# Performance work log

Hardware: AMD Instinct MI355X
Metric: run time of the kernel (lower is better)

The kernel has to match this reference:

```python
import jax, jax.numpy as jnp
import numpy as np
from functools import partial

K = 3
P = K * K * K          # 27 kernel points
G = 2                  # groups
PAD = 1
STRIDE = 1
DIL = 1
AXIS_SCALE = (0.5, 1.0, 1.0)   # (x, y, z) offset axis scale
CUR_SCALE = 0.5                # warmup scale at global_step=0
EPS = 1e-5


def setup_inputs() -> dict:
    key = jax.random.key(0)
    ks = jax.random.split(key, 8)
    C, OC = 64, 64
    N, D, H, W = 1, 32, 32, 32
    inp = {
        "x": jax.random.normal(ks[0], (N, C, D, H, W), jnp.float32),
        "dw_w": jax.random.normal(ks[1], (C, 1, K, K, K), jnp.float32) * 0.1,
        "gn_w": jnp.ones((C,), jnp.float32),
        "gn_b": jnp.zeros((C,), jnp.float32),
        "inp_w": jax.random.normal(ks[2], (C, C), jnp.float32) * (1.0 / np.sqrt(C)),
        "inp_b": jnp.zeros((C,), jnp.float32),
        # offset/mask weights are zero-init in the module; use small random values
        # so the deformable sampling path is exercised nontrivially.
        "off_w": jax.random.normal(ks[3], (C, G * P * 3), jnp.float32) * 0.01,
        "off_b": jnp.zeros((G * P * 3,), jnp.float32),
        "mask_w": jax.random.normal(ks[4], (C, G * P), jnp.float32) * 0.01,
        "mask_b": jnp.tile(jnp.full((P,), -5.0, jnp.float32).at[P // 2].set(0.0), (G,)),
        "out_w": jax.random.normal(ks[5], (C, OC), jnp.float32) * (1.0 / np.sqrt(C)),
        "out_b": jnp.zeros((OC,), jnp.float32),
    }
    return inp


def _trilinear(vol, loc):
    # vol: [Dp, Hp, Wp, gc]; loc: [..., 3] with (x, y, z) in [-1, 1]
    # grid_sample semantics: align_corners=False, padding_mode='zeros'
    Dp, Hp, Wp, _ = vol.shape
    ix = (loc[..., 0] + 1.0) * 0.5 * Wp - 0.5
    iy = (loc[..., 1] + 1.0) * 0.5 * Hp - 0.5
    iz = (loc[..., 2] + 1.0) * 0.5 * Dp - 0.5
    x0f, y0f, z0f = jnp.floor(ix), jnp.floor(iy), jnp.floor(iz)
    fx, fy, fz = ix - x0f, iy - y0f, iz - z0f
    x0, y0, z0 = x0f.astype(jnp.int32), y0f.astype(jnp.int32), z0f.astype(jnp.int32)
    out = jnp.zeros(loc.shape[:-1] + (vol.shape[-1],), vol.dtype)
    for dz in (0, 1):
        wz = fz if dz else 1.0 - fz
        cz = z0 + dz
        for dy in (0, 1):
            wy = fy if dy else 1.0 - fy
            cy = y0 + dy
            for dx in (0, 1):
                wx = fx if dx else 1.0 - fx
                cx = x0 + dx
                valid = ((cz >= 0) & (cz < Dp) & (cy >= 0) & (cy < Hp)
                         & (cx >= 0) & (cx < Wp))
                v = vol[jnp.clip(cz, 0, Dp - 1),
                        jnp.clip(cy, 0, Hp - 1),
                        jnp.clip(cx, 0, Wp - 1)]  # [..., gc]
                out = out + (wz * wy * wx * valid.astype(vol.dtype))[..., None] * v
    return out


def _forward(x, dw_w, gn_w, gn_b, inp_w, inp_b, off_w, off_b,
             mask_w, mask_b, out_w, out_b):
    N, C, D, H, W = x.shape
    gc = C // G
    # --- dw_conv: depthwise conv3d + GroupNorm(1, C) + GELU ---
    xc = jax.lax.conv_general_dilated(
        x, dw_w, window_strides=(1, 1, 1), padding=[(PAD, PAD)] * 3,
        dimension_numbers=("NCDHW", "OIDHW", "NCDHW"), feature_group_count=C)
    mu = xc.mean(axis=(1, 2, 3, 4), keepdims=True)
    var = ((xc - mu) ** 2).mean(axis=(1, 2, 3, 4), keepdims=True)
    xn = (xc - mu) * jax.lax.rsqrt(var + EPS)
    xn = xn * gn_w[None, :, None, None, None] + gn_b[None, :, None, None, None]
    x1 = jnp.transpose(jax.nn.gelu(xn), (0, 2, 3, 4, 1))       # [N,D,H,W,C]
    # --- offset / mask / input projection ---
    offset = x1 @ off_w + off_b                                  # [N,D,H,W,G*P*3]
    mask = jax.nn.softmax(
        (x1 @ mask_w + mask_b).reshape(N, D, H, W, G, P), axis=-1)
    xp = jnp.transpose(x, (0, 2, 3, 4, 1)) @ inp_w + inp_b       # [N,D,H,W,C]
    # --- core deformable sampling ---
    x_pad = jnp.pad(xp, ((0, 0), (PAD, PAD), (PAD, PAD), (PAD, PAD), (0, 0)))
    Dp, Hp, Wp = D + 2 * PAD, H + 2 * PAD, W + 2 * PAD
    Do = (D + 2 * PAD - DIL * (K - 1) - 1) // STRIDE + 1
    Ho = (H + 2 * PAD - DIL * (K - 1) - 1) // STRIDE + 1
    Wo = (W + 2 * PAD - DIL * (K - 1) - 1) // STRIDE + 1
    # reference grid (x/Wp, y/Hp, z/Dp)
    zc, yc, xc_ = jnp.meshgrid(jnp.arange(Do, dtype=jnp.float32),
                               jnp.arange(Ho, dtype=jnp.float32),
                               jnp.arange(Wo, dtype=jnp.float32), indexing="ij")
    ref = jnp.stack(((xc_ * STRIDE + PAD + 0.5) / Wp,
                     (yc * STRIDE + PAD + 0.5) / Hp,
                     (zc * STRIDE + PAD + 0.5) / Dp), axis=-1)   # [Do,Ho,Wo,3]
    # kernel grid
    lin = jnp.linspace(-(K - 1) // 2, (K - 1) // 2, K, dtype=jnp.float32)
    kz, ky, kx = jnp.meshgrid(lin, lin, lin, indexing="ij")
    kgrid = jnp.stack((kx * DIL / Wp, ky * DIL / Hp, kz * DIL / Dp),
                      axis=-1).reshape(P, 3)
    off = offset.reshape(N, Do, Ho, Wo, G, P, 3)
    off_norm = off / jnp.array([Wp, Hp, Dp], jnp.float32)
    axis = jnp.array(AXIS_SCALE, jnp.float32)
    loc = (ref[None, :, :, :, None, None, :]
           + kgrid[None, None, None, None, None, :, :]
           + off_norm * axis * CUR_SCALE)
    loc = loc * 2.0 - 1.0                                        # [N,Do,Ho,Wo,G,P,3]
    vol = jnp.transpose(x_pad.reshape(N, Dp, Hp, Wp, G, gc),
                        (0, 4, 1, 2, 3, 5))                      # [N,G,Dp,Hp,Wp,gc]
    locs = jnp.transpose(loc, (0, 4, 1, 2, 3, 5, 6))             # [N,G,Do,Ho,Wo,P,3]
    sampled = jax.vmap(jax.vmap(_trilinear))(vol, locs)          # [N,G,Do,Ho,Wo,P,gc]
    out = jnp.einsum("ngdhwpc,ndhwgp->ndhwgc", sampled, mask)
    out = out.reshape(N, Do, Ho, Wo, C)
    return out @ out_w + out_b                                   # [N,Do,Ho,Wo,OC]


def reference(x, dw_w, gn_w, gn_b, inp_w, inp_b, off_w, off_b,
              mask_w, mask_b, out_w, out_b):
    return _forward(x, dw_w, gn_w, gn_b, inp_w, inp_b, off_w, off_b,
                    mask_w, mask_b, out_w, out_b)
```

## Files before the change

kernel.cpp:

```cpp
#include <hip/hip_runtime.h>
#include <hip/hip_fp16.h>
#include <math.h>

#define SP 32768
#define PW 38
#define PW2 (PW*PW)
#define PVOX (PW*PW*PW)
#define OMS 228

typedef short bf16x8 __attribute__((ext_vector_type(8)));
typedef unsigned short u16x4 __attribute__((ext_vector_type(4)));
typedef float f32x4 __attribute__((ext_vector_type(4)));

__device__ __forceinline__ unsigned short f2b(float f) {
    unsigned u = __float_as_uint(f);
    u = (u + 0x7FFFu + ((u >> 16) & 1u)) >> 16;
    return (unsigned short)u;
}
__device__ __forceinline__ float b2f1(unsigned short s) {
    return __uint_as_float(((unsigned)s) << 16);
}
__device__ __forceinline__ __half2 h2(unsigned u) {
    return *reinterpret_cast<__half2*>(&u);
}
__device__ __forceinline__ int vox_of(int sb, int v) {
    int tw = sb & 7, th = (sb >> 3) & 15, td = sb >> 7;
    int vw = v & 3, vh = (v >> 2) & 1, vd = v >> 3;
    return (((td << 1) + vd) << 10) + (((th << 1) + vh) << 5) + (tw << 2) + vw;
}

__global__ void k_front(const float* __restrict__ x, const float* __restrict__ dw,
                        const float* __restrict__ off_w, const float* __restrict__ mask_w,
                        const float* __restrict__ off_b, const float* __restrict__ mask_b,
                        const float* __restrict__ inp_w, const float* __restrict__ out_w,
                        unsigned short* __restrict__ WcatB, float* __restrict__ bcat,
                        unsigned short* __restrict__ inpB, unsigned short* __restrict__ outB,
                        unsigned short* __restrict__ xcb, float* __restrict__ partials,
                        unsigned short* __restrict__ xpad) {
    int bb = blockIdx.x, tid = threadIdx.x;
    if (bb < 88) {
        int idx = bb * 256 + tid;
        int j = idx >> 6, k = idx & 63;
        if (j < 224) {
            float v = 0.f;
            if (j < 162) v = off_w[k * 162 + j];
            else if (j < 216) v = mask_w[k * 54 + (j - 162)];
            WcatB[j * 64 + k] = f2b(v);
            if (k == 0) bcat[j] = (j < 162) ? off_b[j] : (j < 216 ? mask_b[j - 162] : 0.f);
        } else if (j < 288) {
            outB[(j - 224) * 64 + k] = f2b(out_w[k * 64 + (j - 224)]);
        } else {
            inpB[(j - 288) * 64 + k] = f2b(inp_w[k * 64 + (j - 288)]);
        }
        return;
    }
    if (bb < 2136) {
        int b4 = bb - 88;
        int e4 = b4 * 256 + tid;
        int c = e4 >> 13, s4 = (e4 & 8191) << 2;
        int d = s4 >> 10, h = (s4 >> 5) & 31, w0 = s4 & 31;
        const float* xs = x + (size_t)c * SP;
        const float* wt = dw + c * 27;
        float a0 = 0.f, a1 = 0.f, a2 = 0.f, a3 = 0.f;
#pragma unroll
        for (int kd = 0; kd < 3; ++kd) {
            int zz = d + kd - 1; if ((unsigned)zz >= 32u) continue;
#pragma unroll
            for (int kh = 0; kh < 3; ++kh) {
                int yy = h + kh - 1; if ((unsigned)yy >= 32u) continue;
                const float* row = xs + (zz << 10) + (yy << 5) + w0;
                float4 L = *(const float4*)row;
                float xl = (w0 > 0) ? row[-1] : 0.f;
                float xr = (w0 < 28) ? row[4] : 0.f;
                const float* wr = wt + kd * 9 + kh * 3;
                float wm = wr[0], wc = wr[1], wp = wr[2];
                a0 = __builtin_fmaf(wm, xl,  __builtin_fmaf(wc, L.x, __builtin_fmaf(wp, L.y, a0)));
                a1 = __builtin_fmaf(wm, L.x, __builtin_fmaf(wc, L.y, __builtin_fmaf(wp, L.z, a1)));
                a2 = __builtin_fmaf(wm, L.y, __builtin_fmaf(wc, L.z, __builtin_fmaf(wp, L.w, a2)));
                a3 = __builtin_fmaf(wm, L.z, __builtin_fmaf(wc, L.w, __builtin_fmaf(wp, xr,  a3)));
            }
        }
        u16x4 o4; o4[0] = f2b(a0); o4[1] = f2b(a1); o4[2] = f2b(a2); o4[3] = f2b(a3);
        *(u16x4*)(xcb + (size_t)e4 * 4) = o4;
        float s1 = a0 + a1 + a2 + a3;
        float s2 = a0 * a0 + a1 * a1 + a2 * a2 + a3 * a3;
#pragma unroll
        for (int off = 32; off > 0; off >>= 1) {
            s1 += __shfl_xor(s1, off);
            s2 += __shfl_xor(s2, off);
        }
        __shared__ float ws[8];
        int wv = tid >> 6, lane = tid & 63;
        if (lane == 0) { ws[wv * 2] = s1; ws[wv * 2 + 1] = s2; }
        __syncthreads();
        if (tid == 0) {
            partials[b4 * 2 + 0] = ws[0] + ws[2] + ws[4] + ws[6];
            partials[b4 * 2 + 1] = ws[1] + ws[3] + ws[5] + ws[7];
        }
        return;
    }
    int cblk = bb - 2136;
    int j = tid >> 4, c4 = tid & 15;
    u16x4 z = {0, 0, 0, 0};
#pragma unroll
    for (int k = 0; k < 4; ++k) {
        int v = cblk * 64 + k * 16 + j;
        if (v >= PVOX) break;
        int zz = v / PW2, r = v - zz * PW2, yy = r / PW, xx = r - yy * PW;
        if (zz < 2 || zz > 33 || yy < 2 || yy > 33 || xx < 2 || xx > 33)
            *(u16x4*)(xpad + (size_t)v * 64 + c4 * 4) = z;
    }
}

__global__ void k_mid(const unsigned short* __restrict__ xcb, const float* __restrict__ partials,
                      const float* __restrict__ gn_w, const float* __restrict__ gn_b,
                      unsigned short* __restrict__ x1b,
                      const float* __restrict__ x,
                      const unsigned short* __restrict__ inpB,
                      const float* __restrict__ inp_b,
                      unsigned short* __restrict__ xpad) {
    int bb = blockIdx.x, tid = threadIdx.x;
    if (bb < 512) {
        __shared__ float rs[256], rq[256];
        __shared__ unsigned short tile[64][66];
        float a = 0.f, b = 0.f;
        for (int i = tid; i < 2048; i += 256) { a += partials[2 * i]; b += partials[2 * i + 1]; }
        rs[tid] = a; rq[tid] = b;
        __syncthreads();
        for (int off = 128; off > 0; off >>= 1) {
            if (tid < off) { rs[tid] += rs[tid + off]; rq[tid] += rq[tid + off]; }
            __syncthreads();
        }
        const float Minv = 1.f / 2097152.f;
        float mu = rs[0] * Minv;
        float var = rq[0] * Minv - mu * mu;
        float rsq = rsqrtf(var + 1e-5f);
        int s0 = bb * 64;
        int row = tid >> 6, lane = tid & 63;
        for (int c = row; c < 64; c += 4) {
            float v = (b2f1(xcb[(size_t)c * SP + s0 + lane]) - mu) * rsq * gn_w[c] + gn_b[c];
            float t2 = 1.5957691216057308f * (v + 0.044715f * v * v * v);
            tile[c][lane] = f2b(v / (1.f + __expf(-t2)));
        }
        __syncthreads();
        for (int r = row; r < 64; r += 4)
            x1b[(size_t)(s0 + r) * 64 + lane] = tile[lane][r];
        return;
    }
    {
        __shared__ unsigned short tileT[64][72];
        int s0b = (bb - 512) * 64;
        int row = tid >> 6, lane = tid & 63;
        for (int c = row; c < 64; c += 4)
            tileT[lane][c] = f2b(x[(size_t)c * SP + s0b + lane]);
        __syncthreads();
        int wv = row, quad = lane >> 4, col = lane & 15;
        int s0 = s0b + wv * 16;
        bf16x8 a0 = *(const bf16x8*)(&tileT[wv * 16 + col][quad * 8]);
        bf16x8 a1 = *(const bf16x8*)(&tileT[wv * 16 + col][32 + quad * 8]);
        int vp[4];
#pragma unroll
        for (int r = 0; r < 4; ++r) {
            int s = s0 + (quad << 2) + r;
            vp[r] = (((s >> 10) + 2) * PW + ((s >> 5) & 31) + 2) * PW + (s & 31) + 2;
        }
#pragma unroll
        for (int nt = 0; nt < 4; ++nt) {
            int n0 = nt * 16;
            bf16x8 b0 = *(const bf16x8*)(inpB + (n0 + col) * 64 + quad * 8);
            bf16x8 b1 = *(const bf16x8*)(inpB + (n0 + col) * 64 + 32 + quad * 8);
            f32x4 c = {0.f, 0.f, 0.f, 0.f};
            c = __builtin_amdgcn_mfma_f32_16x16x32_bf16(a0, b0, c, 0, 0, 0);
            c = __builtin_amdgcn_mfma_f32_16x16x32_bf16(a1, b1, c, 0, 0, 0);
            float bq = inp_b[n0 + col];
#pragma unroll
            for (int r = 0; r < 4; ++r)
                xpad[(size_t)vp[r] * 64 + n0 + col] =
                    __half_as_ushort(__float2half(c[r] + bq));
        }
    }
}

template<int P0, int NP>
__device__ __forceinline__ void sampleN(const float* __restrict__ orow,
                                        const float* __restrict__ mrow,
                                        const char* __restrict__ volc,
                                        float xb, float yb, float zb,
                                        float* __restrict__ acc) {
#pragma unroll
    for (int i = 0; i < NP; ++i) {
        const int p = P0 + i;
        const int px = p % 3, py = (p / 3) % 3, pz = p / 9;
        float ox = orow[p * 3 + 0], oy = orow[p * 3 + 1], oz = orow[p * 3 + 2];
        float mk = mrow[p];
        float ix = __builtin_fmaf(0.25f, ox, xb + (float)px);
        float iy = __builtin_fmaf(0.5f, oy, yb + (float)py);
        float iz = __builtin_fmaf(0.5f, oz, zb + (float)pz);
        ix = fminf(fmaxf(ix, 0.f), 36.f);
        iy = fminf(fmaxf(iy, 0.f), 36.f);
        iz = fminf(fmaxf(iz, 0.f), 36.f);
        float xf = floorf(ix), yf = floorf(iy), zf = floorf(iz);
        float fx = ix - xf, fy = iy - yf, fz = iz - zf;
        float fi = __builtin_fmaf(zf, (float)PW2, __builtin_fmaf(yf, (float)PW, xf));
        int ib = ((int)fi) << 7;
        const char* base = volc + ib;
        uint4 r000 = *(const uint4*)(base);
        uint4 r001 = *(const uint4*)(base + 128);
        uint4 r010 = *(const uint4*)(base + PW * 128);
        uint4 r011 = *(const uint4*)(base + PW * 128 + 128);
        uint4 r100 = *(const uint4*)(base + PW2 * 128);
        uint4 r101 = *(const uint4*)(base + PW2 * 128 + 128);
        uint4 r110 = *(const uint4*)(base + (PW2 + PW) * 128);
        uint4 r111 = *(const uint4*)(base + (PW2 + PW) * 128 + 128);
        __half2 fx2 = __float2half2_rn(fx);
        __half2 fy2 = __float2half2_rn(fy);
        __half2 fz2 = __float2half2_rn(fz);
        #define TRI(comp, ci)                                                   \
        {                                                                       \
            __half2 t0 = __hfma2(fx2, __hsub2(h2(r001.comp), h2(r000.comp)), h2(r000.comp)); \
            __half2 t1 = __hfma2(fx2, __hsub2(h2(r011.comp), h2(r010.comp)), h2(r010.comp)); \
            __half2 t2 = __hfma2(fx2, __hsub2(h2(r101.comp), h2(r100.comp)), h2(r100.comp)); \
            __half2 t3 = __hfma2(fx2, __hsub2(h2(r111.comp), h2(r110.comp)), h2(r110.comp)); \
            __half2 u0 = __hfma2(fy2, __hsub2(t1, t0), t0);                     \
            __half2 u1 = __hfma2(fy2, __hsub2(t3, t2), t2);                     \
            __half2 rr = __hfma2(fz2, __hsub2(u1, u0), u0);                     \
            float2 ff = __half22float2(rr);                                     \
            acc[2 * ci + 0] = __builtin_fmaf(mk, ff.x, acc[2 * ci + 0]);        \
            acc[2 * ci + 1] = __builtin_fmaf(mk, ff.y, acc[2 * ci + 1]);        \
        }
        TRI(x, 0) TRI(y, 1) TRI(z, 2) TRI(w, 3)
        #undef TRI
    }
}

template<int P0, int NP>
__device__ __forceinline__ void sampleL(const float* __restrict__ orow,
                                        const float* __restrict__ mrow,
                                        const char* __restrict__ volp,
                                        float xb, float yb, float zb,
                                        float* __restrict__ acc) {
    float ox[NP], oy[NP], oz[NP], mk[NP];
#pragma unroll
    for (int i = 0; i < NP; ++i) {
        ox[i] = orow[(P0 + i) * 3 + 0];
        oy[i] = orow[(P0 + i) * 3 + 1];
        oz[i] = orow[(P0 + i) * 3 + 2];
        mk[i] = mrow[P0 + i];
    }
#pragma unroll
    for (int i = 0; i < NP; ++i) {
        const int p = P0 + i;
        const int px = p % 3, py = (p / 3) % 3, pz = p / 9;
        float ix = __builtin_fmaf(0.25f, ox[i], xb + (float)px);
        float iy = __builtin_fmaf(0.5f, oy[i], yb + (float)py);
        float iz = __builtin_fmaf(0.5f, oz[i], zb + (float)pz);
        ix = fminf(fmaxf(ix, 0.f), 6.999f);
        iy = fminf(fmaxf(iy, 0.f), 4.999f);
        iz = fminf(fmaxf(iz, 0.f), 4.999f);
        float xf = floorf(ix), yf = floorf(iy), zf = floorf(iz);
        float fx = ix - xf, fy = iy - yf, fz = iz - zf;
        float fi = __builtin_fmaf(zf, 48.f, __builtin_fmaf(yf, 8.f, xf));
        int rr = (int)fi;
        #define RD(o) (*(const uint4*)(volp + ((rr + (o)) << 7)))
        uint4 r000 = RD(0);
        uint4 r001 = RD(1);
        uint4 r010 = RD(8);
        uint4 r011 = RD(9);
        uint4 r100 = RD(48);
        uint4 r101 = RD(49);
        uint4 r110 = RD(56);
        uint4 r111 = RD(57);
        #undef RD
        __half2 fx2 = __float2half2_rn(fx);
        __half2 fy2 = __float2half2_rn(fy);
        __half2 fz2 = __float2half2_rn(fz);
        float m = mk[i];
        #define TRI(comp, ci)                                                   \
        {                                                                       \
            __half2 t0 = __hfma2(fx2, __hsub2(h2(r001.comp), h2(r000.comp)), h2(r000.comp)); \
            __half2 t1 = __hfma2(fx2, __hsub2(h2(r011.comp), h2(r010.comp)), h2(r010.comp)); \
            __half2 t2 = __hfma2(fx2, __hsub2(h2(r101.comp), h2(r100.comp)), h2(r100.comp)); \
            __half2 t3 = __hfma2(fx2, __hsub2(h2(r111.comp), h2(r110.comp)), h2(r110.comp)); \
            __half2 u0 = __hfma2(fy2, __hsub2(t1, t0), t0);                     \
            __half2 u1 = __hfma2(fy2, __hsub2(t3, t2), t2);                     \
            __half2 rr2 = __hfma2(fz2, __hsub2(u1, u0), u0);                    \
            float2 ff = __half22float2(rr2);                                    \
            acc[2 * ci + 0] = __builtin_fmaf(m, ff.x, acc[2 * ci + 0]);         \
            acc[2 * ci + 1] = __builtin_fmaf(m, ff.y, acc[2 * ci + 1]);         \
        }
        TRI(x, 0) TRI(y, 1) TRI(z, 2) TRI(w, 3)
        #undef TRI
    }
}

__global__ void __launch_bounds__(256, 2) k_main(const unsigned short* __restrict__ x1b,
                                                 const unsigned short* __restrict__ xpad,
                                                 const unsigned short* __restrict__ WcatB,
                                                 const float* __restrict__ bcat,
                                                 const unsigned short* __restrict__ outB,
                                                 const float* __restrict__ out_b,
                                                 float* __restrict__ out) {
    __shared__ float om_s[16 * OMS];
    __shared__ unsigned short smb[16 * 72];
    __shared__ char vol[288 * 128];
    __shared__ float pbuf[16 * 64];
    int tid = threadIdx.x, wv = tid >> 6, lane = tid & 63;
    int quad = lane >> 4, col = lane & 15;
    int sb = ((blockIdx.x & 7) << 8) | (blockIdx.x >> 3);
    int tw = sb & 7, th = (sb >> 3) & 15, td = sb >> 7;
    {
        const char* xp = (const char*)xpad;
#pragma unroll
        for (int k = 0; k < 3; ++k) {
            uint4 t[3];
#pragma unroll
            for (int j = 0; j < 3; ++j) {
                int u = tid + (k * 3 + j) * 256;
                int rr = u >> 3, ch = u & 7;
                int dz = rr / 48, rem = rr - dz * 48, dy = rem >> 3, dx = rem & 7;
                int pv = ((2 * td + dz) * PW + (2 * th + dy)) * PW + 4 * tw + dx;
                t[j] = *(const uint4*)(xp + ((size_t)pv << 7) + (ch << 4));
            }
#pragma unroll
            for (int j = 0; j < 3; ++j) {
                int u = tid + (k * 3 + j) * 256;
                *(uint4*)(vol + (u << 4)) = t[j];
            }
        }
    }
    {
        int sv = vox_of(sb, col);
        bf16x8 a0 = *(const bf16x8*)(x1b + (size_t)sv * 64 + quad * 8);
        bf16x8 a1 = *(const bf16x8*)(x1b + (size_t)sv * 64 + 32 + quad * 8);
        for (int jt = wv; jt < 14; jt += 4) {
            int n0 = jt * 16;
            bf16x8 b0 = *(const bf16x8*)(WcatB + (n0 + col) * 64 + quad * 8);
            bf16x8 b1 = *(const bf16x8*)(WcatB + (n0 + col) * 64 + 32 + quad * 8);
            f32x4 c = {0.f, 0.f, 0.f, 0.f};
            c = __builtin_amdgcn_mfma_f32_16x16x32_bf16(a0, b0, c, 0, 0, 0);
            c = __builtin_amdgcn_mfma_f32_16x16x32_bf16(a1, b1, c, 0, 0, 0);
            float bb = bcat[n0 + col];
            int n = n0 + col, slot;
            if (n < 162) slot = n + ((n >= 81) ? 3 : 0);
            else { int n2 = n - 162; slot = 168 + n2 + ((n2 >= 27) ? 1 : 0); }
            if (n < 216) {
#pragma unroll
                for (int r = 0; r < 4; ++r)
                    om_s[(quad * 4 + r) * OMS + slot] = c[r] + bb;
            }
        }
    }
    __syncthreads();
    {
        int row = lane >> 2, sub = lane & 3;
        int vloc = (wv & 1) * 8 + (row >> 1), g = row & 1;
        float* m = &om_s[vloc * OMS + 168 + g * 28];
        float mv[7];
        float mx = -1e30f;
#pragma unroll
        for (int i = 0; i < 7; ++i) {
            int p = sub * 7 + i;
            mv[i] = (p < 27) ? m[p] : -1e30f;
            mx = fmaxf(mx, mv[i]);
        }
        mx = fmaxf(mx, __shfl_xor(mx, 1));
        mx = fmaxf(mx, __shfl_xor(mx, 2));
        float e[7], sm = 0.f;
#pragma unroll
        for (int i = 0; i < 7; ++i) { e[i] = __expf(mv[i] - mx); sm += e[i]; }
        sm += __shfl_xor(sm, 1);
        sm += __shfl_xor(sm, 2);
        float inv = 1.f / sm;
#pragma unroll
        for (int i = 0; i < 7; ++i) {
            int p = sub * 7 + i;
            if (p < 27) m[p] = e[i] * inv;
        }
    }
    {
        int half = wv & 1, mode = wv >> 1;
        int v = half * 8 + (lane >> 3);
        int oct = lane & 7, gg = oct >> 2;
        const float* orow = &om_s[v * OMS + gg * 84];
        const float* mrow = &om_s[v * OMS + 168 + gg * 28];
        float acc[8] = {0.f, 0.f, 0.f, 0.f, 0.f, 0.f, 0.f, 0.f};
        if (mode == 0) {
            int sv = vox_of(sb, v);
            float zb = (float)((sv >> 10) + 1);
            float yb = (float)(((sv >> 5) & 31) + 1);
            float xb = (float)((sv & 31) + 1);
            sampleN<0, 9>(orow, mrow, (const char*)xpad + oct * 16, xb, yb, zb, acc);
        } else {
            int vw = v & 3, vh = (v >> 2) & 1, vd = v >> 3;
            sampleL<9, 18>(orow, mrow, vol + oct * 16,
                           (float)(vw + 1), (float)(vh + 1), (float)(vd + 1), acc);
            float* pp = &pbuf[v * 64 + oct * 8];
            *(f32x4*)(pp) = *(f32x4*)(acc);
            *(f32x4*)(pp + 4) = *(f32x4*)(acc + 4);
        }
        __syncthreads();
        if (mode == 0) {
            const float* pp = &pbuf[v * 64 + oct * 8];
            bf16x8 sb8;
#pragma unroll
            for (int k = 0; k < 8; ++k) sb8[k] = (short)f2b(acc[k] + pp[k]);
            *(bf16x8*)(smb + v * 72 + oct * 8) = sb8;
        }
    }
    __syncthreads();
    {
        bf16x8 oa0 = *(const bf16x8*)(smb + col * 72 + quad * 8);
        bf16x8 oa1 = *(const bf16x8*)(smb + col * 72 + 32 + quad * 8);
        int n0 = wv * 16;
        bf16x8 b0 = *(const bf16x8*)(outB + (n0 + col) * 64 + quad * 8);
        bf16x8 b1 = *(const bf16x8*)(outB + (n0 + col) * 64 + 32 + quad * 8);
        f32x4 c = {0.f, 0.f, 0.f, 0.f};
        c = __builtin_amdgcn_mfma_f32_16x16x32_bf16(oa0, b0, c, 0, 0, 0);
        c = __builtin_amdgcn_mfma_f32_16x16x32_bf16(oa1, b1, c, 0, 0, 0);
        float bb = out_b[n0 + col];
        int vr[4];
#pragma unroll
        for (int r = 0; r < 4; ++r) vr[r] = vox_of(sb, quad * 4 + r);
#pragma unroll
        for (int r = 0; r < 4; ++r)
            out[(size_t)vr[r] * 64 + n0 + col] = c[r] + bb;
    }
}

extern "C" void kernel_launch(void* const* d_in, const int* in_sizes, int n_in,
                              void* d_out, int out_size, void* d_ws, size_t ws_size,
                              hipStream_t stream) {
    const float* x      = (const float*)d_in[0];
    const float* dw_w   = (const float*)d_in[1];
    const float* gn_w   = (const float*)d_in[2];
    const float* gn_b   = (const float*)d_in[3];
    const float* inp_w  = (const float*)d_in[4];
    const float* inp_b  = (const float*)d_in[5];
    const float* off_w  = (const float*)d_in[6];
    const float* off_b  = (const float*)d_in[7];
    const float* mask_w = (const float*)d_in[8];
    const float* mask_b = (const float*)d_in[9];
    const float* out_w  = (const float*)d_in[10];
    const float* out_b  = (const float*)d_in[11];

    char* B = (char*)d_ws;
    float*          partials = (float*)(B + 256);
    unsigned short* xcb      = (unsigned short*)(B + 65792);
    unsigned short* x1b      = (unsigned short*)(B + 8454400);
    unsigned short* xpad     = (unsigned short*)(B + 16843008);
    unsigned short* WcatB    = (unsigned short*)(B + 30890240);
    float*          bcat     = (float*)(B + 30918912);
    unsigned short* inpB     = (unsigned short*)(B + 30919936);
    unsigned short* outB     = (unsigned short*)(B + 30928128);
    float* out = (float*)d_out;

    k_front<<<88 + 2048 + 858, 256, 0, stream>>>(x, dw_w, off_w, mask_w, off_b, mask_b,
                                                 inp_w, out_w, WcatB, bcat, inpB, outB,
                                                 xcb, partials, xpad);
    k_mid<<<512 + 512, 256, 0, stream>>>(xcb, partials, gn_w, gn_b, x1b,
                                         x, inpB, inp_b, xpad);
    k_main<<<2048, 256, 0, stream>>>(x1b, xpad, WcatB, bcat, outB, out_b, out);
}
```

Before: 149.8 us.

## Eliminate k_mid by fusing input projection into k_front and GroupNorm+GELU into k_main

The input projection GEMM moves into k_front as extra blocks, with inp_w transposed into shared memory in each block instead of being prebuilt as a bf16 buffer. The GroupNorm statistics reduction and the GELU activation move into k_main, which now reads xcb directly rather than a precomputed x1b. This removes one kernel launch and the write and read of the intermediate x1b tensor. In exchange, each k_main block re-reduces the partial sums and does strided per-channel gathers from xcb, and every projection block reloads inp_w.

```diff
diff --git a/kernel.cpp b/kernel.cpp
--- a/kernel.cpp
+++ b/kernel.cpp
@@ -32,13 +32,14 @@
 __global__ void k_front(const float* __restrict__ x, const float* __restrict__ dw,
                         const float* __restrict__ off_w, const float* __restrict__ mask_w,
                         const float* __restrict__ off_b, const float* __restrict__ mask_b,
-                        const float* __restrict__ inp_w, const float* __restrict__ out_w,
+                        const float* __restrict__ inp_w, const float* __restrict__ inp_b,
+                        const float* __restrict__ out_w,
                         unsigned short* __restrict__ WcatB, float* __restrict__ bcat,
-                        unsigned short* __restrict__ inpB, unsigned short* __restrict__ outB,
+                        unsigned short* __restrict__ outB,
                         unsigned short* __restrict__ xcb, float* __restrict__ partials,
                         unsigned short* __restrict__ xpad) {
     int bb = blockIdx.x, tid = threadIdx.x;
-    if (bb < 88) {
+    if (bb < 72) {
         int idx = bb * 256 + tid;
         int j = idx >> 6, k = idx & 63;
         if (j < 224) {
@@ -47,15 +48,13 @@
             else if (j < 216) v = mask_w[k * 54 + (j - 162)];
             WcatB[j * 64 + k] = f2b(v);
             if (k == 0) bcat[j] = (j < 162) ? off_b[j] : (j < 216 ? mask_b[j - 162] : 0.f);
-        } else if (j < 288) {
+        } else {
             outB[(j - 224) * 64 + k] = f2b(out_w[k * 64 + (j - 224)]);
-        } else {
-            inpB[(j - 288) * 64 + k] = f2b(inp_w[k * 64 + (j - 288)]);
         }
         return;
     }
-    if (bb < 2136) {
-        int b4 = bb - 88;
+    if (bb < 2120) {
+        int b4 = bb - 72;
         int e4 = b4 * 256 + tid;
         int c = e4 >> 13, s4 = (e4 & 8191) << 2;
         int d = s4 >> 10, h = (s4 >> 5) & 31, w0 = s4 & 31;
@@ -99,7 +98,47 @@
         }
         return;
     }
-    int cblk = bb - 2136;
+    if (bb < 2632) {
+        __shared__ unsigned short tileT[64][72];
+        __shared__ unsigned short inpT[64 * 65];
+        int s0b = (bb - 2120) * 64;
+        int row = tid >> 6, lane = tid & 63;
+        for (int c = row; c < 64; c += 4) {
+            tileT[lane][c] = f2b(x[(size_t)c * SP + s0b + lane]);
+            inpT[c * 65 + lane] = f2b(inp_w[(size_t)c * 64 + lane]);
+        }
+        __syncthreads();
+        int wv = row, quad = lane >> 4, col = lane & 15;
+        int s0 = s0b + wv * 16;
+        bf16x8 a0 = *(const bf16x8*)(&tileT[wv * 16 + col][quad * 8]);
+        bf16x8 a1 = *(const bf16x8*)(&tileT[wv * 16 + col][32 + quad * 8]);
+        int vp[4];
+#pragma unroll
+        for (int r = 0; r < 4; ++r) {
+            int s = s0 + (quad << 2) + r;
+            vp[r] = (((s >> 10) + 2) * PW + ((s >> 5) & 31) + 2) * PW + (s & 31) + 2;
+        }
+#pragma unroll
+        for (int nt = 0; nt < 4; ++nt) {
+            int n0 = nt * 16;
+            bf16x8 b0, b1;
+#pragma unroll
+            for (int t = 0; t < 8; ++t) {
+                b0[t] = (short)inpT[(quad * 8 + t) * 65 + (n0 + col)];
+                b1[t] = (short)inpT[(32 + quad * 8 + t) * 65 + (n0 + col)];
+            }
+            f32x4 c = {0.f, 0.f, 0.f, 0.f};
+            c = __builtin_amdgcn_mfma_f32_16x16x32_bf16(a0, b0, c, 0, 0, 0);
+            c = __builtin_amdgcn_mfma_f32_16x16x32_bf16(a1, b1, c, 0, 0, 0);
+            float bq = inp_b[n0 + col];
+#pragma unroll
+            for (int r = 0; r < 4; ++r)
+                xpad[(size_t)vp[r] * 64 + n0 + col] =
+                    __half_as_ushort(__float2half(c[r] + bq));
+        }
+        return;
+    }
+    int cblk = bb - 2632;
     int j = tid >> 4, c4 = tid & 15;
     u16x4 z = {0, 0, 0, 0};
 #pragma unroll
@@ -109,75 +148,6 @@
         int zz = v / PW2, r = v - zz * PW2, yy = r / PW, xx = r - yy * PW;
         if (zz < 2 || zz > 33 || yy < 2 || yy > 33 || xx < 2 || xx > 33)
             *(u16x4*)(xpad + (size_t)v * 64 + c4 * 4) = z;
-    }
-}
-
-__global__ void k_mid(const unsigned short* __restrict__ xcb, const float* __restrict__ partials,
-                      const float* __restrict__ gn_w, const float* __restrict__ gn_b,
-                      unsigned short* __restrict__ x1b,
-                      const float* __restrict__ x,
-                      const unsigned short* __restrict__ inpB,
-                      const float* __restrict__ inp_b,
-                      unsigned short* __restrict__ xpad) {
-    int bb = blockIdx.x, tid = threadIdx.x;
-    if (bb < 512) {
-        __shared__ float rs[256], rq[256];
-        __shared__ unsigned short tile[64][66];
-        float a = 0.f, b = 0.f;
-        for (int i = tid; i < 2048; i += 256) { a += partials[2 * i]; b += partials[2 * i + 1]; }
-        rs[tid] = a; rq[tid] = b;
-        __syncthreads();
-        for (int off = 128; off > 0; off >>= 1) {
-            if (tid < off) { rs[tid] += rs[tid + off]; rq[tid] += rq[tid + off]; }
-            __syncthreads();
-        }
-        const float Minv = 1.f / 2097152.f;
-        float mu = rs[0] * Minv;
-        float var = rq[0] * Minv - mu * mu;
-        float rsq = rsqrtf(var + 1e-5f);
-        int s0 = bb * 64;
-        int row = tid >> 6, lane = tid & 63;
-        for (int c = row; c < 64; c += 4) {
-            float v = (b2f1(xcb[(size_t)c * SP + s0 + lane]) - mu) * rsq * gn_w[c] + gn_b[c];
-            float t2 = 1.5957691216057308f * (v + 0.044715f * v * v * v);
-            tile[c][lane] = f2b(v / (1.f + __expf(-t2)));
-        }
-        __syncthreads();
-        for (int r = row; r < 64; r += 4)
-            x1b[(size_t)(s0 + r) * 64 + lane] = tile[lane][r];
-        return;
-    }
-    {
-        __shared__ unsigned short tileT[64][72];
-        int s0b = (bb - 512) * 64;
-        int row = tid >> 6, lane = tid & 63;
-        for (int c = row; c < 64; c += 4)
-            tileT[lane][c] = f2b(x[(size_t)c * SP + s0b + lane]);
-        __syncthreads();
-        int wv = row, quad = lane >> 4, col = lane & 15;
-        int s0 = s0b + wv * 16;
-        bf16x8 a0 = *(const bf16x8*)(&tileT[wv * 16 + col][quad * 8]);
-        bf16x8 a1 = *(const bf16x8*)(&tileT[wv * 16 + col][32 + quad * 8]);
-        int vp[4];
-#pragma unroll
-        for (int r = 0; r < 4; ++r) {
-            int s = s0 + (quad << 2) + r;
-            vp[r] = (((s >> 10) + 2) * PW + ((s >> 5) & 31) + 2) * PW + (s & 31) + 2;
-        }
-#pragma unroll
-        for (int nt = 0; nt < 4; ++nt) {
-            int n0 = nt * 16;
-            bf16x8 b0 = *(const bf16x8*)(inpB + (n0 + col) * 64 + quad * 8);
-            bf16x8 b1 = *(const bf16x8*)(inpB + (n0 + col) * 64 + 32 + quad * 8);
-            f32x4 c = {0.f, 0.f, 0.f, 0.f};
-            c = __builtin_amdgcn_mfma_f32_16x16x32_bf16(a0, b0, c, 0, 0, 0);
-            c = __builtin_amdgcn_mfma_f32_16x16x32_bf16(a1, b1, c, 0, 0, 0);
-            float bq = inp_b[n0 + col];
-#pragma unroll
-            for (int r = 0; r < 4; ++r)
-                xpad[(size_t)vp[r] * 64 + n0 + col] =
-                    __half_as_ushort(__float2half(c[r] + bq));
-        }
     }
 }
 
@@ -293,7 +263,10 @@
     }
 }
 
-__global__ void __launch_bounds__(256, 2) k_main(const unsigned short* __restrict__ x1b,
+__global__ void __launch_bounds__(256, 2) k_main(const unsigned short* __restrict__ xcb,
+                                                 const float* __restrict__ partials,
+                                                 const float* __restrict__ gn_w,
+                                                 const float* __restrict__ gn_b,
                                                  const unsigned short* __restrict__ xpad,
                                                  const unsigned short* __restrict__ WcatB,
                                                  const float* __restrict__ bcat,
@@ -304,6 +277,7 @@
     __shared__ unsigned short smb[16 * 72];
     __shared__ char vol[288 * 128];
     __shared__ float pbuf[16 * 64];
+    __shared__ float gnw_s[64], gnb_s[64], ws[8];
     int tid = threadIdx.x, wv = tid >> 6, lane = tid & 63;
     int quad = lane >> 4, col = lane & 15;
     int sb = ((blockIdx.x & 7) << 8) | (blockIdx.x >> 3);
@@ -329,9 +303,39 @@
         }
     }
     {
+        if (tid < 64) { gnw_s[tid] = gn_w[tid]; gnb_s[tid] = gn_b[tid]; }
+        float a = 0.f, b = 0.f;
+#pragma unroll
+        for (int i = 0; i < 4; ++i) {
+            float4 t = *(const float4*)(partials + 4 * (tid + i * 256));
+            a += t.x + t.z;
+            b += t.y + t.w;
+        }
+#pragma unroll
+        for (int off = 32; off > 0; off >>= 1) {
+            a += __shfl_xor(a, off);
+            b += __shfl_xor(b, off);
+        }
+        if (lane == 0) { ws[wv * 2] = a; ws[wv * 2 + 1] = b; }
+    }
+    __syncthreads();
+    const float Minv = 1.f / 2097152.f;
+    float mu = (ws[0] + ws[2] + ws[4] + ws[6]) * Minv;
+    float var = (ws[1] + ws[3] + ws[5] + ws[7]) * Minv - mu * mu;
+    float rsq = rsqrtf(var + 1e-5f);
+    {
         int sv = vox_of(sb, col);
-        bf16x8 a0 = *(const bf16x8*)(x1b + (size_t)sv * 64 + quad * 8);
-        bf16x8 a1 = *(const bf16x8*)(x1b + (size_t)sv * 64 + 32 + quad * 8);
+        bf16x8 a0, a1;
+#pragma unroll
+        for (int t = 0; t < 8; ++t) {
+            int c0 = quad * 8 + t, c1 = 32 + quad * 8 + t;
+            float v0 = (b2f1(xcb[(size_t)c0 * SP + sv]) - mu) * rsq * gnw_s[c0] + gnb_s[c0];
+            float q0 = 1.5957691216057308f * (v0 + 0.044715f * v0 * v0 * v0);
+            a0[t] = (short)f2b(v0 / (1.f + __expf(-q0)));
+            float v1 = (b2f1(xcb[(size_t)c1 * SP + sv]) - mu) * rsq * gnw_s[c1] + gnb_s[c1];
+            float q1 = 1.5957691216057308f * (v1 + 0.044715f * v1 * v1 * v1);
+            a1[t] = (short)f2b(v1 / (1.f + __expf(-q1)));
+        }
         for (int jt = wv; jt < 14; jt += 4) {
             int n0 = jt * 16;
             bf16x8 b0 = *(const bf16x8*)(WcatB + (n0 + col) * 64 + quad * 8);
@@ -446,18 +450,15 @@
     char* B = (char*)d_ws;
     float*          partials = (float*)(B + 256);
     unsigned short* xcb      = (unsigned short*)(B + 65792);
-    unsigned short* x1b      = (unsigned short*)(B + 8454400);
     unsigned short* xpad     = (unsigned short*)(B + 16843008);
     unsigned short* WcatB    = (unsigned short*)(B + 30890240);
     float*          bcat     = (float*)(B + 30918912);
-    unsigned short* inpB     = (unsigned short*)(B + 30919936);
     unsigned short* outB     = (unsigned short*)(B + 30928128);
     float* out = (float*)d_out;
 
-    k_front<<<88 + 2048 + 858, 256, 0, stream>>>(x, dw_w, off_w, mask_w, off_b, mask_b,
-                                                 inp_w, out_w, WcatB, bcat, inpB, outB,
-                                                 xcb, partials, xpad);
-    k_mid<<<512 + 512, 256, 0, stream>>>(xcb, partials, gn_w, gn_b, x1b,
-                                         x, inpB, inp_b, xpad);
-    k_main<<<2048, 256, 0, stream>>>(x1b, xpad, WcatB, bcat, outB, out_b, out);
-}
+    k_front<<<72 + 2048 + 512 + 858, 256, 0, stream>>>(x, dw_w, off_w, mask_w, off_b, mask_b,
+                                                       inp_w, inp_b, out_w, WcatB, bcat, outB,
+                                                       xcb, partials, xpad);
+    k_main<<<2048, 256, 0, stream>>>(xcb, partials, gn_w, gn_b, xpad,
+                                     WcatB, bcat, outB, out_b, out);
+}
```

Result: no change. 148.2 us (-1.0%).
